# Optimization experiments

Hardware: AMD Instinct MI355X
Metric: run time of the kernel (lower is better)

The kernel has to match this reference:

```python
import jax, jax.numpy as jnp
import numpy as np


def setup_inputs() -> dict:
    key = jax.random.key(0)
    x = jax.random.normal(key, (32, 1024, 1024), dtype=jnp.float32)
    return {"x": x}


def reference(x) -> jnp.ndarray:
    # Orthonormal DCT-II along axis 1 via length-2n FFT of [x, reverse(x)],
    # matching tf dct_odd_case numerics (complex64 path, real part taken).
    N, n, m = x.shape
    nf = jnp.float32(n)
    # y = [x; flip(x, axis=1)] -> length 2n along axis 1
    y = jnp.concatenate([x, x[:, ::-1, :]], axis=1)
    F = jnp.fft.fft(y.astype(jnp.complex64), axis=1)[:, :n, :]  # [N, n, m] complex64
    k = jnp.arange(n, dtype=jnp.float32)
    # twiddle: exp(-i*pi*k/(2n)) / sqrt(2n), with k=0 term divided by sqrt(2)
    phase = -k * (jnp.pi / (2.0 * nf))
    t = (jnp.cos(phase) + 1j * jnp.sin(phase)).astype(jnp.complex64) / jnp.sqrt(2.0 * nf)
    scale0 = jnp.where(k == 0, 1.0 / jnp.sqrt(jnp.float32(2.0)), jnp.float32(1.0))
    t = t * scale0.astype(jnp.complex64)
    dct_x = jnp.real(t[None, :, None] * F)  # [N, n, m] float32
    return dct_x
```

## Files before the change

### kernel.cpp

```cpp
#include <hip/hip_runtime.h>
#include <hip/hip_bf16.h>
#include <math.h>

typedef __bf16 bf16_8 __attribute__((ext_vector_type(8)));
typedef float f32x4 __attribute__((ext_vector_type(4)));

#define NDIM 1024
#define BM 128
#define BN 128
#define BK 32
#define BSTRIDE 40

__device__ static inline void async_copy16(const void* g, void* l) {
  __builtin_amdgcn_global_load_lds(
      (__attribute__((address_space(1))) void*)g,
      (__attribute__((address_space(3))) void*)l, 16, 0, 0);
}

__global__ void gen_dct_mat(__bf16* __restrict__ C) {
  int idx = blockIdx.x * blockDim.x + threadIdx.x;
  int k = idx >> 10;
  int j = idx & 1023;
  int t = (k * (2 * j + 1)) & 4095;
  float ang = (float)t * 1.5339807878856412e-3f;
  float s = (k == 0) ? 0.03125f : 0.04419417382415922f;
  C[idx] = (__bf16)(s * cosf(ang));
}

__global__ __launch_bounds__(256) void dct_gemm(
    const float* __restrict__ x, const __bf16* __restrict__ A,
    float* __restrict__ out) {
  __shared__ __align__(64) __bf16 Asm[BM * BK];
  __shared__ __align__(64) __bf16 Bsm[BN * BSTRIDE];

  const int t = threadIdx.x;
  const int wave = t >> 6;
  const int lane = t & 63;
  const int bb = blockIdx.z;
  const int m0 = blockIdx.y * BM;
  const int n0 = blockIdx.x * BN;

  const __bf16* Ag0 =
      A + (size_t)(m0 + wave * 16 + (lane >> 2)) * NDIM + ((lane & 3) * 8);
  const __bf16* Ag1 = Ag0 + (size_t)64 * NDIM;
  __bf16* Al0 = Asm + (wave * 16) * BK;
  __bf16* Al1 = Asm + (64 + wave * 16) * BK;

  const int bc = t & 127;
  const int bjg = t >> 7;
  const float* xs =
      x + (size_t)bb * (NDIM * NDIM) + (size_t)(bjg * 16) * NDIM + (n0 + bc);
  bf16_8* bs0 = (bf16_8*)(Bsm + bc * BSTRIDE + bjg * 16);
  bf16_8* bs1 = (bf16_8*)(Bsm + bc * BSTRIDE + bjg * 16 + 8);

  const int row16 = lane & 15;
  const int kq8 = (lane >> 4) * 8;
  const int wm = (wave & 1) * 64;
  const int wn = (wave >> 1) * 64;

  f32x4 acc[4][4] = {};

  for (int k0 = 0; k0 < NDIM; k0 += BK) {
    __syncthreads();
    async_copy16(Ag0 + k0, Al0);
    async_copy16(Ag1 + k0, Al1);

    const float* xp = xs + (size_t)k0 * NDIM;
    bf16_8 v0, v1;
#pragma unroll
    for (int q = 0; q < 8; q++) {
      v0[q] = (__bf16)xp[(size_t)q * NDIM];
      v1[q] = (__bf16)xp[(size_t)(q + 8) * NDIM];
    }
    *bs0 = v0;
    *bs1 = v1;
    __syncthreads();

    bf16_8 af[4], bfr[4];
#pragma unroll
    for (int i = 0; i < 4; i++)
      af[i] = *(const bf16_8*)(Asm + (wm + i * 16 + row16) * BK + kq8);
#pragma unroll
    for (int j = 0; j < 4; j++)
      bfr[j] = *(const bf16_8*)(Bsm + (wn + j * 16 + row16) * BSTRIDE + kq8);
#pragma unroll
    for (int i = 0; i < 4; i++)
#pragma unroll
      for (int j = 0; j < 4; j++)
        acc[i][j] = __builtin_amdgcn_mfma_f32_16x16x32_bf16(af[i], bfr[j],
                                                            acc[i][j], 0, 0, 0);
  }

  float* ob = out + (size_t)bb * (NDIM * NDIM);
  const int rbase = (lane >> 4) * 4;
  const int cofs = lane & 15;
#pragma unroll
  for (int i = 0; i < 4; i++) {
#pragma unroll
    for (int r = 0; r < 4; r++) {
      int row = m0 + wm + i * 16 + rbase + r;
#pragma unroll
      for (int j = 0; j < 4; j++) {
        int col = n0 + wn + j * 16 + cofs;
        ob[(size_t)row * NDIM + col] = acc[i][j][r];
      }
    }
  }
}

extern "C" void kernel_launch(void* const* d_in, const int* in_sizes, int n_in,
                              void* d_out, int out_size, void* d_ws,
                              size_t ws_size, hipStream_t stream) {
  const float* x = (const float*)d_in[0];
  float* out = (float*)d_out;
  __bf16* Cmat = (__bf16*)d_ws;

  gen_dct_mat<<<dim3((NDIM * NDIM) / 256), dim3(256), 0, stream>>>(Cmat);

  dim3 grid(NDIM / BN, NDIM / BM, 32);
  dct_gemm<<<grid, dim3(256), 0, stream>>>(x, Cmat, out);
}
```

Before: 304.2 us.

## Pre-transpose input to blocked swizzled bf16 and double-buffer the GEMM

Adds a separate kernel that converts x to bf16 and transposes it into tile-blocked, XOR-swizzled 64-wide K panels. The DCT matrix is generated in the same blocked layout. A new GEMM then streams both operands with async global-to-LDS copies into double-buffered shared memory, using BK=64 and bank-conflict-free swizzled reads. This removes the strided per-element fp32 loads and conversions from the GEMM inner loop. In exchange it adds an extra pass that writes and rereads a 64 MB bf16 workspace, and it needs a large workspace, falling back to the old path when the workspace is too small.

```diff
diff --git a/kernel.cpp b/kernel.cpp
--- a/kernel.cpp
+++ b/kernel.cpp
@@ -6,16 +6,149 @@
 typedef float f32x4 __attribute__((ext_vector_type(4)));
 
 #define NDIM 1024
+
+__device__ static inline void async_copy16(const void* g, void* l) {
+  __builtin_amdgcn_global_load_lds(
+      (__attribute__((address_space(1))) void*)g,
+      (__attribute__((address_space(3))) void*)l, 16, 0, 0);
+}
+
+
+__global__ void gen_dct_blocked(__bf16* __restrict__ A) {
+  int idx = blockIdx.x * blockDim.x + threadIdx.x;
+  int m = idx >> 7;
+  int ks = idx & 127;
+  int kt = ks >> 3, s = ks & 7;
+  int mt = m >> 7, r = m & 127;
+  float sc = (m == 0) ? 0.03125f : 0.04419417382415922f;
+  int kbase = kt * 64 + s * 8;
+  bf16_8 v;
+#pragma unroll
+  for (int q = 0; q < 8; q++) {
+    int k = kbase + q;
+    int t = (m * (2 * k + 1)) & 4095;
+    float ang = (float)t * 1.5339807878856412e-3f;
+    v[q] = (__bf16)(sc * cosf(ang));
+  }
+  *(bf16_8*)(A + (((size_t)(mt * 16 + kt)) << 13) + r * 64 + ((s ^ (r & 7)) << 3)) = v;
+}
+
+#define TP 132
+__global__ __launch_bounds__(256) void transpose_cvt(const float* __restrict__ x,
+                                                     __bf16* __restrict__ B) {
+  __shared__ float T[64 * TP];
+  const int t = threadIdx.x;
+  const int kt = blockIdx.x, nt = blockIdx.y, b = blockIdx.z;
+  const float* xb =
+      x + (size_t)b * (NDIM * NDIM) + (size_t)kt * 64 * NDIM + nt * 128;
+  {
+    const int kr = t >> 5;
+    const int c4 = (t & 31) * 4;
+#pragma unroll
+    for (int u = 0; u < 8; u++) {
+      int k = u * 8 + kr;
+      f32x4 v = *(const f32x4*)(xb + (size_t)k * NDIM + c4);
+      *(f32x4*)(&T[k * TP + c4]) = v;
+    }
+  }
+  __syncthreads();
+  __bf16* img = B + (((size_t)((b * 8 + nt) * 16 + kt)) << 13);
+#pragma unroll
+  for (int u = 0; u < 4; u++) {
+    int c = t * 4 + u;
+    int r = c >> 3, sp = c & 7;
+    int s = sp ^ (r & 7);
+    bf16_8 v;
+#pragma unroll
+    for (int q = 0; q < 8; q++) v[q] = (__bf16)T[(s * 8 + q) * TP + r];
+    *(bf16_8*)(img + c * 8) = v;
+  }
+}
+
+__global__ __launch_bounds__(256) void dct_gemm2(const __bf16* __restrict__ A,
+                                                 const __bf16* __restrict__ B,
+                                                 float* __restrict__ out) {
+  __shared__ __align__(1024) __bf16 As[2][128 * 64];
+  __shared__ __align__(1024) __bf16 Bs[2][128 * 64];
+  const int t = threadIdx.x;
+  const int w = t >> 6, lane = t & 63;
+  const int nt = blockIdx.x, mt = blockIdx.y, b = blockIdx.z;
+
+  const __bf16* ag = A + (((size_t)mt * 16) << 13) + w * 2048 + lane * 8;
+  const __bf16* bg =
+      B + (((size_t)((b * 8 + nt) * 16)) << 13) + w * 2048 + lane * 8;
+
+  const int r16 = lane & 15;
+  const int g8 = (lane >> 4) << 3;
+  const int wm = (w & 1) << 6, wn = (w >> 1) << 6;
+  const int xr = (r16 & 7) << 3;
+  const int kof0 = g8 ^ xr;
+  const int kof1 = (32 + g8) ^ xr;
+
+#pragma unroll
+  for (int i = 0; i < 4; i++) {
+    async_copy16(ag + i * 512, &As[0][w * 2048 + i * 512]);
+    async_copy16(bg + i * 512, &Bs[0][w * 2048 + i * 512]);
+  }
+  __syncthreads();
+
+  f32x4 acc[4][4] = {};
+
+  for (int kt = 0; kt < 16; kt++) {
+    const int cur = kt & 1;
+    if (kt < 15) {
+      const __bf16* an = ag + (size_t)(kt + 1) * 8192;
+      const __bf16* bn = bg + (size_t)(kt + 1) * 8192;
+      const int nb = cur ^ 1;
+#pragma unroll
+      for (int i = 0; i < 4; i++) {
+        async_copy16(an + i * 512, &As[nb][w * 2048 + i * 512]);
+        async_copy16(bn + i * 512, &Bs[nb][w * 2048 + i * 512]);
+      }
+    }
+    const __bf16* as = &As[cur][0];
+    const __bf16* bs = &Bs[cur][0];
+#pragma unroll
+    for (int h = 0; h < 2; h++) {
+      const int kof = h ? kof1 : kof0;
+      bf16_8 af[4], bfr[4];
+#pragma unroll
+      for (int i = 0; i < 4; i++)
+        af[i] = *(const bf16_8*)(as + (wm + i * 16 + r16) * 64 + kof);
+#pragma unroll
+      for (int j = 0; j < 4; j++)
+        bfr[j] = *(const bf16_8*)(bs + (wn + j * 16 + r16) * 64 + kof);
+#pragma unroll
+      for (int i = 0; i < 4; i++)
+#pragma unroll
+        for (int j = 0; j < 4; j++)
+          acc[i][j] = __builtin_amdgcn_mfma_f32_16x16x32_bf16(af[i], bfr[j],
+                                                              acc[i][j], 0, 0, 0);
+    }
+    __syncthreads();
+  }
+
+  float* ob = out + (size_t)b * (NDIM * NDIM);
+  const int rbase = (lane >> 4) << 2;
+  const int cofs = lane & 15;
+  const int m0 = mt * 128, n0 = nt * 128;
+#pragma unroll
+  for (int i = 0; i < 4; i++)
+#pragma unroll
+    for (int rr = 0; rr < 4; rr++) {
+      int row = m0 + wm + i * 16 + rbase + rr;
+#pragma unroll
+      for (int j = 0; j < 4; j++) {
+        int col = n0 + wn + j * 16 + cofs;
+        ob[(size_t)row * NDIM + col] = acc[i][j][rr];
+      }
+    }
+}
+
 #define BM 128
 #define BN 128
 #define BK 32
 #define BSTRIDE 40
-
-__device__ static inline void async_copy16(const void* g, void* l) {
-  __builtin_amdgcn_global_load_lds(
-      (__attribute__((address_space(1))) void*)g,
-      (__attribute__((address_space(3))) void*)l, 16, 0, 0);
-}
 
 __global__ void gen_dct_mat(__bf16* __restrict__ C) {
   int idx = blockIdx.x * blockDim.x + threadIdx.x;
@@ -113,10 +246,18 @@
                               size_t ws_size, hipStream_t stream) {
   const float* x = (const float*)d_in[0];
   float* out = (float*)d_out;
-  __bf16* Cmat = (__bf16*)d_ws;
-
-  gen_dct_mat<<<dim3((NDIM * NDIM) / 256), dim3(256), 0, stream>>>(Cmat);
-
-  dim3 grid(NDIM / BN, NDIM / BM, 32);
-  dct_gemm<<<grid, dim3(256), 0, stream>>>(x, Cmat, out);
-}
+
+  const size_t need = (size_t)66 * 1024 * 1024;
+  if (ws_size >= need) {
+    __bf16* Ab = (__bf16*)d_ws;
+    __bf16* Bb = Ab + (size_t)1024 * 1024;
+    gen_dct_blocked<<<dim3(512), dim3(256), 0, stream>>>(Ab);
+    transpose_cvt<<<dim3(16, 8, 32), dim3(256), 0, stream>>>(x, Bb);
+    dct_gemm2<<<dim3(8, 8, 32), dim3(256), 0, stream>>>(Ab, Bb, out);
+  } else {
+    __bf16* Cmat = (__bf16*)d_ws;
+    gen_dct_mat<<<dim3((NDIM * NDIM) / 256), dim3(256), 0, stream>>>(Cmat);
+    dct_gemm<<<dim3(NDIM / BN, NDIM / BM, 32), dim3(256), 0, stream>>>(x, Cmat,
+                                                                       out);
+  }
+}
```

New measurement: 302.2 us. No clear change (-0.6%).
